# Kernel optimization log

Measured on AMD Instinct MI355X. Metric: run time of the kernel, lower is better.

Reference implementation:

```python
import jax, jax.numpy as jnp
import numpy as np

B, L, D, MAXL = 4, 2048, 1024, 4096

def setup_inputs() -> dict:
    key = jax.random.key(0)
    ks = jax.random.split(key, 7)
    x = jax.random.normal(ks[0], (B, L, D), dtype=jnp.float32)
    mask = jnp.ones((B, 1, L), dtype=jnp.int32)
    # kv_proj: Linear(D,D) -> ReLU -> Linear(D, 2D)
    s1 = 1.0 / np.sqrt(D)
    W1 = jax.random.uniform(ks[1], (D, D), minval=-s1, maxval=s1, dtype=jnp.float32)
    b1 = jax.random.uniform(ks[2], (D,), minval=-s1, maxval=s1, dtype=jnp.float32)
    W2 = jax.random.uniform(ks[3], (D, 2 * D), minval=-s1, maxval=s1, dtype=jnp.float32)
    b2 = jax.random.uniform(ks[4], (2 * D,), minval=-s1, maxval=s1, dtype=jnp.float32)
    D_to_L = jax.random.normal(ks[5], (D, MAXL), dtype=jnp.float32) * 0.01
    return {"x": x, "mask": mask, "W1": W1, "b1": b1, "W2": W2, "b2": b2, "D_to_L": D_to_L}

def reference(x, mask, W1, b1, W2, b2, D_to_L):
    Lcur = x.shape[1]
    h = jax.nn.relu(x @ W1 + b1)          # [B,L,D]
    kv = h @ W2 + b2                       # [B,L,2D]
    k, value = jnp.split(kv, 2, axis=-1)   # [B,L,D] each
    scores = jnp.einsum('bld,dk->blk', k, D_to_L[:, :Lcur])  # [B,L,L]
    scores = jnp.where(mask == 0, -jnp.inf, scores)
    attention = jax.nn.softmax(scores, axis=-1)
    output = attention @ value             # [B,L,D]
    return output, attention
```

## Files before the change

### kernel.cpp

```cpp
#include <hip/hip_runtime.h>
#include <cstdint>
#include <cstddef>

__device__ __forceinline__ float bf2f(uint16_t u) {
    union { uint32_t i; float f; } w; w.i = ((uint32_t)u) << 16; return w.f;
}
__device__ __forceinline__ uint16_t f2bf(float f) {
    union { float f; uint32_t i; } w; w.f = f;
    uint32_t x = w.i;
    uint32_t r = (x + 0x7FFFu + ((x >> 16) & 1u)) >> 16;
    return (uint16_t)r;
}

typedef __bf16 bf16x8 __attribute__((ext_vector_type(8)));
typedef float  f32x4  __attribute__((ext_vector_type(4)));

__device__ __forceinline__ void load_lds16(const void* gptr, void* lptr) {
    __builtin_amdgcn_global_load_lds(
        (__attribute__((address_space(1))) void*)gptr,
        (__attribute__((address_space(3))) void*)lptr,
        16, 0, 0);
}

template<int AFP32, int OUTFP32, int RELU>
__global__ __launch_bounds__(256, 3)
void gemm_bt(const void* __restrict__ Av, const uint16_t* __restrict__ BT,
             const float* __restrict__ bias, void* __restrict__ Cv,
             int K, int lda, int ldb, int ldc,
             long long sA, long long sB, long long sC)
{
    __shared__ uint16_t As[128 * 32];
    __shared__ uint16_t Bs[128 * 32];

    const int t    = threadIdx.x;
    const int lane = t & 63;
    const int w    = t >> 6;
    const int quad = lane >> 4;
    const int l15  = lane & 15;
    const int wr   = w >> 1;
    const int wc   = w & 1;
    const int gm0  = blockIdx.y * 128;
    const int gn0  = blockIdx.x * 128;

    BT += (long long)blockIdx.z * sB;

    f32x4 acc[4][4] = {};

    const int ch_r = lane >> 2;
    const int ch_c = (lane & 3) * 8;

    for (int k0 = 0; k0 < K; k0 += 32) {
        __syncthreads();

        {
            int row = w * 16 + ch_r;
            load_lds16(BT + (size_t)(gn0 + row) * ldb + k0 + ch_c, (void*)(Bs + w * 512));
            load_lds16(BT + (size_t)(gn0 + row + 64) * ldb + k0 + ch_c, (void*)(Bs + (w + 4) * 512));
        }
        if (AFP32) {
            const float* A = (const float*)Av + (long long)blockIdx.z * sA;
            const int row = t >> 1, half = t & 1;
            const float* ap = A + (size_t)(gm0 + row) * lda + k0 + half * 16;
            float4 f0 = ((const float4*)ap)[0];
            float4 f1 = ((const float4*)ap)[1];
            float4 f2 = ((const float4*)ap)[2];
            float4 f3 = ((const float4*)ap)[3];
            uint32_t p[8];
            p[0] = (uint32_t)f2bf(f0.x) | ((uint32_t)f2bf(f0.y) << 16);
            p[1] = (uint32_t)f2bf(f0.z) | ((uint32_t)f2bf(f0.w) << 16);
            p[2] = (uint32_t)f2bf(f1.x) | ((uint32_t)f2bf(f1.y) << 16);
            p[3] = (uint32_t)f2bf(f1.z) | ((uint32_t)f2bf(f1.w) << 16);
            p[4] = (uint32_t)f2bf(f2.x) | ((uint32_t)f2bf(f2.y) << 16);
            p[5] = (uint32_t)f2bf(f2.z) | ((uint32_t)f2bf(f2.w) << 16);
            p[6] = (uint32_t)f2bf(f3.x) | ((uint32_t)f2bf(f3.y) << 16);
            p[7] = (uint32_t)f2bf(f3.z) | ((uint32_t)f2bf(f3.w) << 16);
            uint4* d = (uint4*)(As + row * 32 + half * 16);
            d[0] = make_uint4(p[0], p[1], p[2], p[3]);
            d[1] = make_uint4(p[4], p[5], p[6], p[7]);
        } else {
            const uint16_t* A = (const uint16_t*)Av + (long long)blockIdx.z * sA;
            int row = w * 16 + ch_r;
            load_lds16(A + (size_t)(gm0 + row) * lda + k0 + ch_c, (void*)(As + w * 512));
            load_lds16(A + (size_t)(gm0 + row + 64) * lda + k0 + ch_c, (void*)(As + (w + 4) * 512));
        }
        __syncthreads();

        bf16x8 af[4], bfr[4];
#pragma unroll
        for (int i = 0; i < 4; i++) {
            af[i]  = *(const bf16x8*)(As + (wr * 64 + i * 16 + l15) * 32 + quad * 8);
            bfr[i] = *(const bf16x8*)(Bs + (wc * 64 + i * 16 + l15) * 32 + quad * 8);
        }
#pragma unroll
        for (int mi = 0; mi < 4; mi++)
#pragma unroll
            for (int ni = 0; ni < 4; ni++)
                acc[mi][ni] = __builtin_amdgcn_mfma_f32_16x16x32_bf16(af[mi], bfr[ni], acc[mi][ni], 0, 0, 0);
    }

#pragma unroll
    for (int ni = 0; ni < 4; ni++) {
        const int gcol = gn0 + wc * 64 + ni * 16 + l15;
        const float bv = bias ? bias[gcol] : 0.0f;
#pragma unroll
        for (int mi = 0; mi < 4; mi++) {
#pragma unroll
            for (int r = 0; r < 4; r++) {
                const int grow = gm0 + wr * 64 + mi * 16 + quad * 4 + r;
                float v = acc[mi][ni][r] + bv;
                if (RELU) v = fmaxf(v, 0.0f);
                if (OUTFP32) {
                    float* C = (float*)Cv + (long long)blockIdx.z * sC;
                    C[(size_t)grow * ldc + gcol] = v;
                } else {
                    uint16_t* C = (uint16_t*)Cv + (long long)blockIdx.z * sC;
                    C[(size_t)grow * ldc + gcol] = f2bf(v);
                }
            }
        }
    }
}

__global__ __launch_bounds__(256)
void transpose_f32_to_bf16(const float* __restrict__ src, uint16_t* __restrict__ dst,
                           int src_ld, int dst_ld)
{
    __shared__ uint16_t tile[64 * 65];
    const int k0 = blockIdx.y * 64, n0 = blockIdx.x * 64;
    const int t = threadIdx.x;
#pragma unroll
    for (int i = 0; i < 16; i++) {
        int idx = i * 256 + t;
        int r = idx >> 6, c = idx & 63;
        tile[c * 65 + r] = f2bf(src[(size_t)(k0 + r) * src_ld + n0 + c]);
    }
    __syncthreads();
#pragma unroll
    for (int i = 0; i < 16; i++) {
        int idx = i * 256 + t;
        int n = idx >> 6, k = idx & 63;
        dst[(size_t)(n0 + n) * dst_ld + k0 + k] = tile[n * 65 + k];
    }
}

__global__ __launch_bounds__(256)
void transpose_bf16(const uint16_t* __restrict__ src, uint16_t* __restrict__ dst,
                    int src_ld, int dst_ld, long long sS, long long sD)
{
    __shared__ uint16_t tile[64 * 65];
    src += (long long)blockIdx.z * sS;
    dst += (long long)blockIdx.z * sD;
    const int k0 = blockIdx.y * 64, n0 = blockIdx.x * 64;
    const int t = threadIdx.x;
#pragma unroll
    for (int i = 0; i < 16; i++) {
        int idx = i * 256 + t;
        int r = idx >> 6, c = idx & 63;
        tile[c * 65 + r] = src[(size_t)(k0 + r) * src_ld + n0 + c];
    }
    __syncthreads();
#pragma unroll
    for (int i = 0; i < 16; i++) {
        int idx = i * 256 + t;
        int n = idx >> 6, k = idx & 63;
        dst[(size_t)(n0 + n) * dst_ld + k0 + k] = tile[n * 65 + k];
    }
}

__global__ __launch_bounds__(256)
void softmax_rows_f32(float* __restrict__ S, const int* __restrict__ mask, int L)
{
    const int row = blockIdx.x;
    const int b = row >> 11;
    float* rp = S + (size_t)row * L;
    const int* mrow = mask + (size_t)b * L;
    const int t = threadIdx.x;
    const int c0 = t * 8;

    float v[8];
    *(float4*)(v + 0) = *(const float4*)(rp + c0);
    *(float4*)(v + 4) = *(const float4*)(rp + c0 + 4);
    bool mk[8];
    float lmax = -1e30f;
#pragma unroll
    for (int j = 0; j < 8; j++) {
        mk[j] = (mrow[c0 + j] != 0);
        if (mk[j]) lmax = fmaxf(lmax, v[j]);
    }
#pragma unroll
    for (int off = 32; off > 0; off >>= 1)
        lmax = fmaxf(lmax, __shfl_xor(lmax, off, 64));

    __shared__ float redm[4];
    __shared__ float reds[4];
    const int w = t >> 6, lane = t & 63;
    if (lane == 0) redm[w] = lmax;
    __syncthreads();
    lmax = fmaxf(fmaxf(redm[0], redm[1]), fmaxf(redm[2], redm[3]));

    float e[8];
    float lsum = 0.f;
#pragma unroll
    for (int j = 0; j < 8; j++) {
        e[j] = mk[j] ? __expf(v[j] - lmax) : 0.0f;
        lsum += e[j];
    }
#pragma unroll
    for (int off = 32; off > 0; off >>= 1)
        lsum += __shfl_xor(lsum, off, 64);
    if (lane == 0) reds[w] = lsum;
    __syncthreads();
    lsum = reds[0] + reds[1] + reds[2] + reds[3];

    const float inv = 1.0f / lsum;
#pragma unroll
    for (int j = 0; j < 8; j++) v[j] = e[j] * inv;
    *(float4*)(rp + c0)     = *(const float4*)(v + 0);
    *(float4*)(rp + c0 + 4) = *(const float4*)(v + 4);
}

extern "C" void kernel_launch(void* const* d_in, const int* in_sizes, int n_in,
                              void* d_out, int out_size, void* d_ws, size_t ws_size,
                              hipStream_t stream)
{
    const float* x    = (const float*)d_in[0];
    const int*   mask = (const int*)d_in[1];
    const float* W1   = (const float*)d_in[2];
    const float* b1   = (const float*)d_in[3];
    const float* W2   = (const float*)d_in[4];
    const float* b2   = (const float*)d_in[5];
    const float* D2L  = (const float*)d_in[6];

    const int Lr = 2048, D = 1024, M = 4 * Lr;
    float* outp = (float*)d_out;
    float* attn = outp + (size_t)M * D;

    uint16_t* W1T  = (uint16_t*)d_ws;
    uint16_t* W2T  = W1T + 1024 * 1024;
    uint16_t* D2LT = W2T + 2048 * 1024;
    uint16_t* hbuf = D2LT + 2048 * 1024;
    uint16_t* kv   = hbuf + (size_t)M * D;
    uint16_t* vT   = hbuf;

    dim3 blk(256);

    transpose_f32_to_bf16<<<dim3(16, 16), blk, 0, stream>>>(W1,  W1T,  1024, 1024);
    transpose_f32_to_bf16<<<dim3(32, 16), blk, 0, stream>>>(W2,  W2T,  2048, 1024);
    transpose_f32_to_bf16<<<dim3(32, 16), blk, 0, stream>>>(D2L, D2LT, 4096, 1024);

    gemm_bt<1, 0, 1><<<dim3(8, 64, 1), blk, 0, stream>>>(x, W1T, b1, hbuf,
        1024, 1024, 1024, 1024, 0, 0, 0);

    gemm_bt<0, 0, 0><<<dim3(16, 64, 1), blk, 0, stream>>>(hbuf, W2T, b2, kv,
        1024, 1024, 1024, 2048, 0, 0, 0);

    transpose_bf16<<<dim3(16, 32, 4), blk, 0, stream>>>(kv + 1024, vT,
        2048, 2048, (long long)2048 * 2048, (long long)1024 * 2048);

    gemm_bt<0, 1, 0><<<dim3(16, 64, 1), blk, 0, stream>>>(kv, D2LT, nullptr, attn,
        1024, 2048, 1024, 2048, 0, 0, 0);

    softmax_rows_f32<<<dim3(8192), blk, 0, stream>>>(attn, mask, Lr);

    gemm_bt<1, 1, 0><<<dim3(8, 16, 4), blk, 0, stream>>>(attn, vT, nullptr, outp,
        2048, 2048, 2048, 1024,
        (long long)2048 * 2048, (long long)1024 * 2048, (long long)2048 * 1024);
}
```

Measured before the change: 390.4 us.

## Emit bf16 attention copy from softmax, remap GEMM blocks per XCD, use native bf16 casts

```diff
diff --git a/kernel.cpp b/kernel.cpp
--- a/kernel.cpp
+++ b/kernel.cpp
@@ -31,6 +31,17 @@
 {
     __shared__ uint16_t As[128 * 32];
     __shared__ uint16_t Bs[128 * 32];
+
+    const int nx = (int)gridDim.x, ny = (int)gridDim.y, nz = (int)gridDim.z;
+    const int g   = (int)blockIdx.x + nx * ((int)blockIdx.y + ny * (int)blockIdx.z);
+    const int xcd = g & 7;
+    const int ii  = g >> 3;
+    const int xz  = 8 / nz;
+    const int bz  = xcd / xz;
+    const int sub = xcd % xz;
+    const int ypc = ny / xz;
+    const int by  = sub * ypc + ii % ypc;
+    const int bx  = ii / ypc;
 
     const int t    = threadIdx.x;
     const int lane = t & 63;
@@ -39,10 +50,10 @@
     const int l15  = lane & 15;
     const int wr   = w >> 1;
     const int wc   = w & 1;
-    const int gm0  = blockIdx.y * 128;
-    const int gn0  = blockIdx.x * 128;
-
-    BT += (long long)blockIdx.z * sB;
+    const int gm0  = by * 128;
+    const int gn0  = bx * 128;
+
+    BT += (long long)bz * sB;
 
     f32x4 acc[4][4] = {};
 
@@ -58,27 +69,27 @@
             load_lds16(BT + (size_t)(gn0 + row + 64) * ldb + k0 + ch_c, (void*)(Bs + (w + 4) * 512));
         }
         if (AFP32) {
-            const float* A = (const float*)Av + (long long)blockIdx.z * sA;
+            const float* A = (const float*)Av + (long long)bz * sA;
             const int row = t >> 1, half = t & 1;
             const float* ap = A + (size_t)(gm0 + row) * lda + k0 + half * 16;
             float4 f0 = ((const float4*)ap)[0];
             float4 f1 = ((const float4*)ap)[1];
             float4 f2 = ((const float4*)ap)[2];
             float4 f3 = ((const float4*)ap)[3];
-            uint32_t p[8];
-            p[0] = (uint32_t)f2bf(f0.x) | ((uint32_t)f2bf(f0.y) << 16);
-            p[1] = (uint32_t)f2bf(f0.z) | ((uint32_t)f2bf(f0.w) << 16);
-            p[2] = (uint32_t)f2bf(f1.x) | ((uint32_t)f2bf(f1.y) << 16);
-            p[3] = (uint32_t)f2bf(f1.z) | ((uint32_t)f2bf(f1.w) << 16);
-            p[4] = (uint32_t)f2bf(f2.x) | ((uint32_t)f2bf(f2.y) << 16);
-            p[5] = (uint32_t)f2bf(f2.z) | ((uint32_t)f2bf(f2.w) << 16);
-            p[6] = (uint32_t)f2bf(f3.x) | ((uint32_t)f2bf(f3.y) << 16);
-            p[7] = (uint32_t)f2bf(f3.z) | ((uint32_t)f2bf(f3.w) << 16);
+            union { __bf16 h[16]; uint4 q[2]; } u;
+            u.h[0]  = (__bf16)f0.x; u.h[1]  = (__bf16)f0.y;
+            u.h[2]  = (__bf16)f0.z; u.h[3]  = (__bf16)f0.w;
+            u.h[4]  = (__bf16)f1.x; u.h[5]  = (__bf16)f1.y;
+            u.h[6]  = (__bf16)f1.z; u.h[7]  = (__bf16)f1.w;
+            u.h[8]  = (__bf16)f2.x; u.h[9]  = (__bf16)f2.y;
+            u.h[10] = (__bf16)f2.z; u.h[11] = (__bf16)f2.w;
+            u.h[12] = (__bf16)f3.x; u.h[13] = (__bf16)f3.y;
+            u.h[14] = (__bf16)f3.z; u.h[15] = (__bf16)f3.w;
             uint4* d = (uint4*)(As + row * 32 + half * 16);
-            d[0] = make_uint4(p[0], p[1], p[2], p[3]);
-            d[1] = make_uint4(p[4], p[5], p[6], p[7]);
+            d[0] = u.q[0];
+            d[1] = u.q[1];
         } else {
-            const uint16_t* A = (const uint16_t*)Av + (long long)blockIdx.z * sA;
+            const uint16_t* A = (const uint16_t*)Av + (long long)bz * sA;
             int row = w * 16 + ch_r;
             load_lds16(A + (size_t)(gm0 + row) * lda + k0 + ch_c, (void*)(As + w * 512));
             load_lds16(A + (size_t)(gm0 + row + 64) * lda + k0 + ch_c, (void*)(As + (w + 4) * 512));
@@ -110,10 +121,10 @@
                 float v = acc[mi][ni][r] + bv;
                 if (RELU) v = fmaxf(v, 0.0f);
                 if (OUTFP32) {
-                    float* C = (float*)Cv + (long long)blockIdx.z * sC;
+                    float* C = (float*)Cv + (long long)bz * sC;
                     C[(size_t)grow * ldc + gcol] = v;
                 } else {
-                    uint16_t* C = (uint16_t*)Cv + (long long)blockIdx.z * sC;
+                    uint16_t* C = (uint16_t*)Cv + (long long)bz * sC;
                     C[(size_t)grow * ldc + gcol] = f2bf(v);
                 }
             }
@@ -168,11 +179,13 @@
 }
 
 __global__ __launch_bounds__(256)
-void softmax_rows_f32(float* __restrict__ S, const int* __restrict__ mask, int L)
+void softmax_rows_f32(float* __restrict__ S, uint16_t* __restrict__ Sbf,
+                      const int* __restrict__ mask, int L)
 {
     const int row = blockIdx.x;
     const int b = row >> 11;
     float* rp = S + (size_t)row * L;
+    uint16_t* bp = Sbf + (size_t)row * L;
     const int* mrow = mask + (size_t)b * L;
     const int t = threadIdx.x;
     const int c0 = t * 8;
@@ -213,10 +226,15 @@
     lsum = reds[0] + reds[1] + reds[2] + reds[3];
 
     const float inv = 1.0f / lsum;
-#pragma unroll
-    for (int j = 0; j < 8; j++) v[j] = e[j] * inv;
+    uint16_t ub[8];
+#pragma unroll
+    for (int j = 0; j < 8; j++) {
+        v[j] = e[j] * inv;
+        ub[j] = f2bf(v[j]);
+    }
     *(float4*)(rp + c0)     = *(const float4*)(v + 0);
     *(float4*)(rp + c0 + 4) = *(const float4*)(v + 4);
+    *(uint4*)(bp + c0)      = *(const uint4*)ub;
 }
 
 extern "C" void kernel_launch(void* const* d_in, const int* in_sizes, int n_in,
@@ -241,6 +259,7 @@
     uint16_t* hbuf = D2LT + 2048 * 1024;
     uint16_t* kv   = hbuf + (size_t)M * D;
     uint16_t* vT   = hbuf;
+    uint16_t* abf  = kv;
 
     dim3 blk(256);
 
@@ -260,9 +279,9 @@
     gemm_bt<0, 1, 0><<<dim3(16, 64, 1), blk, 0, stream>>>(kv, D2LT, nullptr, attn,
         1024, 2048, 1024, 2048, 0, 0, 0);
 
-    softmax_rows_f32<<<dim3(8192), blk, 0, stream>>>(attn, mask, Lr);
-
-    gemm_bt<1, 1, 0><<<dim3(8, 16, 4), blk, 0, stream>>>(attn, vT, nullptr, outp,
+    softmax_rows_f32<<<dim3(8192), blk, 0, stream>>>(attn, abf, mask, Lr);
+
+    gemm_bt<0, 1, 0><<<dim3(8, 16, 4), blk, 0, stream>>>(abf, vT, nullptr, outp,
         2048, 2048, 2048, 1024,
         (long long)2048 * 2048, (long long)1024 * 2048, (long long)2048 * 1024);
 }
```

New measurement: 359.1 us. 8.0% less time.
